# Optimization experiments

Hardware: AMD Instinct MI355X
Metric: run time of the kernel (lower is better)

Reference implementation:

```python
import jax, jax.numpy as jnp
import numpy as np

# ---- sizes ----
VOCAB, D = 272, 512
B, S = 8, 8192
# ---- token ids (bytes are 0..255; specials above) ----
CODE_START, CODE_END, MEM, THINK_START, THINK_END = 256, 257, 258, 259, 260
# ---- embedding dim layout (from docstrings: ADDR_KEY dims 206-253, MEM_STORE 455) ----
ADDR_KEY, MEM_STORE, MARK_TS, MARK_TE, MEM_EXEC = 206, 455, 456, 457, 458
INSTR_WIDTH, PC_OFFSET, BYTES_PER_INSTR, DATA_BYTES = 8, 2, 8, 5


def setup_inputs() -> dict:
    key = jax.random.key(0)
    k1, k2 = jax.random.split(key)
    token_ids = jax.random.randint(k1, (B, S), 0, VOCAB, dtype=jnp.int32)
    embed_table = jax.random.normal(k2, (VOCAB, D), dtype=jnp.float32) * 0.02
    return {"embed_table": embed_table, "token_ids": token_ids}


def _addr_onehots(addr, mask):
    """addr: [B,S] int (only low 12 bits used), mask: [B,S] bool -> [B,S,48] bool
    one-hot of lo nibble (0-15), hi nibble (16-31), top nibble (32-47)."""
    r = jnp.arange(16, dtype=jnp.int32)
    lo = r == (addr & 15)[..., None]
    hi = r == ((addr >> 4) & 15)[..., None]
    top = r == ((addr >> 8) & 15)[..., None]
    return jnp.concatenate([lo, hi, top], axis=-1) & mask[..., None]


def reference(embed_table, token_ids):
    x = embed_table[token_ids]  # [B,S,D] gather
    Bq, Sq = token_ids.shape
    idx = jnp.arange(Sq, dtype=jnp.int32)[None, :]  # [1,S]

    # --- _add_code_addr_keys: positions after most-recent CODE_START, before first CODE_END ---
    is_cs = token_ids == CODE_START
    is_ce = token_ids == CODE_END
    first_ce = jnp.min(jnp.where(is_ce, idx, Sq), axis=1)  # [B]
    cs_pos = jax.lax.cummax(jnp.where(is_cs, idx, -1), axis=1)  # [B,S] latest CODE_START <= i
    seq_pos = idx - cs_pos - 1
    byte_off = seq_pos % BYTES_PER_INSTR
    code_mask = ((cs_pos >= 0) & (idx < first_ce[:, None]) & (token_ids < 256)
                 & (seq_pos >= 0) & (byte_off < DATA_BYTES))
    code_addr = (seq_pos // BYTES_PER_INSTR) * INSTR_WIDTH + PC_OFFSET + byte_off
    oh48 = _addr_onehots(code_addr & 0xFFF, code_mask)  # [B,S,48]

    # MEM section: [MEM, addr_b0..addr_b3, val_b0..val_b3]; only low 12 addr bits matter
    tp = jnp.pad(token_ids, ((0, 0), (0, 8)))
    addr12 = (tp[:, 1:Sq + 1] | (tp[:, 2:Sq + 2] << 8)) & 0xFFF  # little-endian, low 12 bits
    mem_mask = (token_ids == MEM) & ((idx + 8) < Sq)  # [B,S]
    for off in range(4):  # val byte positions i+5+off get ADDR_KEY = addr+off
        sh = 5 + off
        m = jnp.pad(mem_mask, ((0, 0), (sh, 0)))[:, :Sq]
        a = jnp.pad(addr12, ((0, 0), (sh, 0)))[:, :Sq] + off
        oh48 = oh48 | _addr_onehots(a & 0xFFF, m)

    # scatter writes (set-to-1.0 semantics)
    ak = x[:, :, ADDR_KEY:ADDR_KEY + 48]
    x = x.at[:, :, ADDR_KEY:ADDR_KEY + 48].set(jnp.where(oh48, 1.0, ak))
    x = x.at[:, :, MEM_EXEC].set(jnp.where(mem_mask, 1.0, x[:, :, MEM_EXEC]))
    # --- _inject_thinking_markers ---
    x = x.at[:, :, MARK_TS].set(jnp.where(token_ids == THINK_START, 1.0, x[:, :, MARK_TS]))
    x = x.at[:, :, MARK_TE].set(jnp.where(token_ids == THINK_END, 1.0, x[:, :, MARK_TE]))
    # _inject_mem_store skipped (_mem_history_end == 0 at construction);
    # _inject_active_opcode skipped (active_opcode=None default).
    return x
```

## Files before the change

### kernel.cpp

```cpp
#include <hip/hip_runtime.h>
#include <stdint.h>

#define BB 8
#define SS 8192
#define DD 512

#define TOK_CS 256
#define TOK_CE 257
#define TOK_MEM 258
#define TOK_TS 259
#define TOK_TE 260

typedef float vfloat4 __attribute__((ext_vector_type(4)));

__global__ __launch_bounds__(256) void meta_kernel(const int* __restrict__ tokens,
                                                   unsigned long long* __restrict__ meta) {
    __shared__ int t[SS];
    __shared__ int chunkmax[256];
    __shared__ int cemin_sh[256];

    const int b = blockIdx.x;
    const int tid = threadIdx.x;
    const int* rt = tokens + (size_t)b * SS;

    int cemin = SS;
    for (int i = tid; i < SS; i += 256) {
        int v = rt[i];
        t[i] = v;
        if (v == TOK_CE && i < cemin) cemin = i;
    }
    cemin_sh[tid] = cemin;
    __syncthreads();
    for (int off = 128; off > 0; off >>= 1) {
        if (tid < off) {
            int o = cemin_sh[tid + off];
            if (o < cemin_sh[tid]) cemin_sh[tid] = o;
        }
        __syncthreads();
    }
    const int first_ce = cemin_sh[0];

    const int c0 = tid * 32;
    int cm = -1;
    for (int i = c0; i < c0 + 32; ++i)
        if (t[i] == TOK_CS) cm = i;
    chunkmax[tid] = cm;
    __syncthreads();

    int carry = -1;
    for (int c = 0; c < tid; ++c) {
        int v = chunkmax[c];
        if (v > carry) carry = v;
    }

    unsigned long long* mrow = meta + (size_t)b * SS;
    int cs = carry;
    for (int i = c0; i < c0 + 32; ++i) {
        const int v = t[i];
        if (v == TOK_CS) cs = i;

        unsigned long long m = ((unsigned long long)v) << 52;

        if (cs >= 0 && i < first_ce && v < 256) {
            int sp = i - cs - 1;
            if (sp >= 0) {
                int bo = sp & 7;
                if (bo < 5) {
                    int addr = ((sp >> 3) << 3) + 2 + bo;
                    addr &= 4095;
                    m |= (1ull << (addr & 15))
                       | (1ull << (16 + ((addr >> 4) & 15)))
                       | (1ull << (32 + ((addr >> 8) & 15)));
                }
            }
        }

        #pragma unroll
        for (int off = 0; off < 4; ++off) {
            int jj = i - 5 - off;
            if (jj >= 0 && (jj + 8) < SS && t[jj] == TOK_MEM) {
                int a = ((t[jj + 1] | (t[jj + 2] << 8)) & 4095) + off;
                a &= 4095;
                m |= (1ull << (a & 15))
                   | (1ull << (16 + ((a >> 4) & 15)))
                   | (1ull << (32 + ((a >> 8) & 15)));
            }
        }

        if (v == TOK_TS) m |= (1ull << 48);
        if (v == TOK_TE) m |= (1ull << 49);
        if (v == TOK_MEM && (i + 8) < SS) m |= (1ull << 50);

        mrow[i] = m;
    }
}

__global__ __launch_bounds__(256) void write_kernel(const vfloat4* __restrict__ embed4,
                                                    const unsigned long long* __restrict__ meta,
                                                    vfloat4* __restrict__ out) {
    const int gid = blockIdx.x * 256 + threadIdx.x;
    const int pos = gid >> 7;
    const int k = gid & 127;

    const unsigned long long m = meta[pos];
    const int tok = (int)(m >> 52);

    vfloat4 v = embed4[tok * 128 + k];

    if (k >= 51 && k <= 63) {
        const int d0 = k * 4;
        #pragma unroll
        for (int j = 0; j < 4; ++j) {
            int r = d0 + j - 206;
            if (r >= 0 && r < 48 && ((m >> r) & 1ull)) v[j] = 1.0f;
        }
    } else if (k == 114) {
        #pragma unroll
        for (int j = 0; j < 3; ++j) {
            if ((m >> (48 + j)) & 1ull) v[j] = 1.0f;
        }
    }

    __builtin_nontemporal_store(v, &out[(size_t)pos * 128 + k]);
}

extern "C" void kernel_launch(void* const* d_in, const int* in_sizes, int n_in,
                              void* d_out, int out_size, void* d_ws, size_t ws_size,
                              hipStream_t stream) {
    const float* embed = (const float*)d_in[0];
    const int* tokens = (const int*)d_in[1];
    unsigned long long* meta = (unsigned long long*)d_ws;

    meta_kernel<<<BB, 256, 0, stream>>>(tokens, meta);

    const int total_f4 = BB * SS * (DD / 4);
    write_kernel<<<total_f4 / 256, 256, 0, stream>>>(
        (const vfloat4*)embed, meta, (vfloat4*)d_out);
}
```

Before: 176.3 us.

## Fuse metadata and write kernels into one segmented kernel with prefix carry

Replaces the two-kernel pipeline (8-block metadata pass followed by a write pass) with one kernel of 512 blocks. Each block handles 128 positions. It recomputes the CODE_START/CODE_END carry by scanning the row prefix before its segment, then runs a wave-level shuffle scan inside the segment. The per-position metadata stays in LDS and is consumed directly by the write loop. This removes a serial, low-parallelism 8-block kernel, a launch and the global metadata round trip, at the cost of redundant prefix reads of tokens (quadratic in segments, up to 8K ints per block).

```diff
diff --git a/kernel.cpp b/kernel.cpp
--- a/kernel.cpp
+++ b/kernel.cpp
@@ -11,58 +11,85 @@
 #define TOK_TS 259
 #define TOK_TE 260
 
+#define SEGS 64
+#define PB 128
+
 typedef float vfloat4 __attribute__((ext_vector_type(4)));
 
-__global__ __launch_bounds__(256) void meta_kernel(const int* __restrict__ tokens,
-                                                   unsigned long long* __restrict__ meta) {
-    __shared__ int t[SS];
-    __shared__ int chunkmax[256];
-    __shared__ int cemin_sh[256];
+__global__ __launch_bounds__(256) void fused_kernel(const int* __restrict__ tokens,
+                                                    const vfloat4* __restrict__ embed4,
+                                                    vfloat4* __restrict__ out) {
+    __shared__ int tloc[PB + 8];
+    __shared__ unsigned long long mlds[PB];
+    __shared__ int rcs[256];
+    __shared__ int rce[256];
+    __shared__ int wtot_cs, wtot_ce;
 
-    const int b = blockIdx.x;
+    const int blk = blockIdx.x;
+    const int row = blk >> 6;
+    const int seg = blk & 63;
+    const int start = seg * PB;
     const int tid = threadIdx.x;
-    const int* rt = tokens + (size_t)b * SS;
+    const int* rt = tokens + (size_t)row * SS;
 
-    int cemin = SS;
-    for (int i = tid; i < SS; i += 256) {
-        int v = rt[i];
-        t[i] = v;
-        if (v == TOK_CE && i < cemin) cemin = i;
+    int maxcs = -1, anyce = 0;
+    for (int j = tid; j < start; j += 256) {
+        int v = rt[j];
+        if (v == TOK_CS) maxcs = j;
+        if (v == TOK_CE) anyce = 1;
     }
-    cemin_sh[tid] = cemin;
+    rcs[tid] = maxcs;
+    rce[tid] = anyce;
+
+    for (int h = tid; h < PB + 8; h += 256) {
+        int g = start - 8 + h;
+        tloc[h] = (g >= 0) ? rt[g] : 0;
+    }
     __syncthreads();
     for (int off = 128; off > 0; off >>= 1) {
         if (tid < off) {
-            int o = cemin_sh[tid + off];
-            if (o < cemin_sh[tid]) cemin_sh[tid] = o;
+            int a = rcs[tid + off];
+            if (a > rcs[tid]) rcs[tid] = a;
+            rce[tid] |= rce[tid + off];
         }
         __syncthreads();
     }
-    const int first_ce = cemin_sh[0];
+    const int carry_cs = rcs[0];
+    const int carry_ce = rce[0];
 
-    const int c0 = tid * 32;
-    int cm = -1;
-    for (int i = c0; i < c0 + 32; ++i)
-        if (t[i] == TOK_CS) cm = i;
-    chunkmax[tid] = cm;
+    int myv = 0, cs_scan = -1, ce_scan = 0;
+    if (tid < PB) {
+        myv = tloc[8 + tid];
+        cs_scan = (myv == TOK_CS) ? (start + tid) : -1;
+        ce_scan = (myv == TOK_CE) ? 1 : 0;
+    }
+    const int lane = tid & 63;
+    #pragma unroll
+    for (int off = 1; off < 64; off <<= 1) {
+        int u = __shfl_up(cs_scan, off);
+        int w = __shfl_up(ce_scan, off);
+        if (lane >= off) {
+            if (u > cs_scan) cs_scan = u;
+            ce_scan |= w;
+        }
+    }
+    if (tid == 63) { wtot_cs = cs_scan; wtot_ce = ce_scan; }
     __syncthreads();
-
-    int carry = -1;
-    for (int c = 0; c < tid; ++c) {
-        int v = chunkmax[c];
-        if (v > carry) carry = v;
+    if (tid >= 64 && tid < PB) {
+        if (wtot_cs > cs_scan) cs_scan = wtot_cs;
+        ce_scan |= wtot_ce;
     }
 
-    unsigned long long* mrow = meta + (size_t)b * SS;
-    int cs = carry;
-    for (int i = c0; i < c0 + 32; ++i) {
-        const int v = t[i];
-        if (v == TOK_CS) cs = i;
+    if (tid < PB) {
+        if (carry_cs > cs_scan) cs_scan = carry_cs;
+        ce_scan |= carry_ce;
 
+        const int i = start + tid;
+        const int v = myv;
         unsigned long long m = ((unsigned long long)v) << 52;
 
-        if (cs >= 0 && i < first_ce && v < 256) {
-            int sp = i - cs - 1;
+        if (cs_scan >= 0 && ce_scan == 0 && v < 256) {
+            int sp = i - cs_scan - 1;
             if (sp >= 0) {
                 int bo = sp & 7;
                 if (bo < 5) {
@@ -78,8 +105,9 @@
         #pragma unroll
         for (int off = 0; off < 4; ++off) {
             int jj = i - 5 - off;
-            if (jj >= 0 && (jj + 8) < SS && t[jj] == TOK_MEM) {
-                int a = ((t[jj + 1] | (t[jj + 2] << 8)) & 4095) + off;
+            int lj = jj - start + 8;
+            if (jj >= 0 && (jj + 8) < SS && tloc[lj] == TOK_MEM) {
+                int a = ((tloc[lj + 1] | (tloc[lj + 2] << 8)) & 4095) + off;
                 a &= 4095;
                 m |= (1ull << (a & 15))
                    | (1ull << (16 + ((a >> 4) & 15)))
@@ -91,37 +119,38 @@
         if (v == TOK_TE) m |= (1ull << 49);
         if (v == TOK_MEM && (i + 8) < SS) m |= (1ull << 50);
 
-        mrow[i] = m;
+        mlds[tid] = m;
     }
-}
+    __syncthreads();
 
-__global__ __launch_bounds__(256) void write_kernel(const vfloat4* __restrict__ embed4,
-                                                    const unsigned long long* __restrict__ meta,
-                                                    vfloat4* __restrict__ out) {
-    const int gid = blockIdx.x * 256 + threadIdx.x;
-    const int pos = gid >> 7;
-    const int k = gid & 127;
+    const int k = tid & 127;
+    const int half = tid >> 7;
+    vfloat4* orow = out + ((size_t)row * SS + start) * 128;
 
-    const unsigned long long m = meta[pos];
-    const int tok = (int)(m >> 52);
+    #pragma unroll 4
+    for (int it = 0; it < PB / 2; ++it) {
+        const int pl = it * 2 + half;
+        const unsigned long long m = mlds[pl];
+        const int tok = (int)(m >> 52);
 
-    vfloat4 v = embed4[tok * 128 + k];
+        vfloat4 v = embed4[tok * 128 + k];
 
-    if (k >= 51 && k <= 63) {
-        const int d0 = k * 4;
-        #pragma unroll
-        for (int j = 0; j < 4; ++j) {
-            int r = d0 + j - 206;
-            if (r >= 0 && r < 48 && ((m >> r) & 1ull)) v[j] = 1.0f;
+        if (k >= 51 && k <= 63) {
+            const int d0 = k * 4;
+            #pragma unroll
+            for (int j = 0; j < 4; ++j) {
+                int r = d0 + j - 206;
+                if (r >= 0 && r < 48 && ((m >> r) & 1ull)) v[j] = 1.0f;
+            }
+        } else if (k == 114) {
+            #pragma unroll
+            for (int j = 0; j < 3; ++j) {
+                if ((m >> (48 + j)) & 1ull) v[j] = 1.0f;
+            }
         }
-    } else if (k == 114) {
-        #pragma unroll
-        for (int j = 0; j < 3; ++j) {
-            if ((m >> (48 + j)) & 1ull) v[j] = 1.0f;
-        }
+
+        __builtin_nontemporal_store(v, &orow[pl * 128 + k]);
     }
-
-    __builtin_nontemporal_store(v, &out[(size_t)pos * 128 + k]);
 }
 
 extern "C" void kernel_launch(void* const* d_in, const int* in_sizes, int n_in,
@@ -129,11 +158,7 @@
                               hipStream_t stream) {
     const float* embed = (const float*)d_in[0];
     const int* tokens = (const int*)d_in[1];
-    unsigned long long* meta = (unsigned long long*)d_ws;
 
-    meta_kernel<<<BB, 256, 0, stream>>>(tokens, meta);
-
-    const int total_f4 = BB * SS * (DD / 4);
-    write_kernel<<<total_f4 / 256, 256, 0, stream>>>(
-        (const vfloat4*)embed, meta, (vfloat4*)d_out);
+    fused_kernel<<<BB * SEGS, 256, 0, stream>>>(
+        tokens, (const vfloat4*)embed, (vfloat4*)d_out);
 }
```

Measured after the change: 154.5 us. -12.4%, faster.
